# Performance work log

Hardware: AMD Instinct MI355X
Metric: run time of the kernel (lower is better)

The kernel has to match this reference:

```python
import jax, jax.numpy as jnp
import numpy as np

N_GROUP = 64
GROUP_SIZE = 64
INPUT_DIM = 2048
BATCH = 8192
N_MONTN = 512


def setup_inputs() -> dict:
    key = jax.random.key(0)
    k1, k2, k3, k4, k5 = jax.random.split(key, 5)
    x = jax.random.normal(k1, (BATCH, INPUT_DIM), dtype=jnp.float32)
    weight = jax.random.normal(k2, (N_GROUP * GROUP_SIZE, INPUT_DIM), dtype=jnp.float32) * 0.02
    bias = jax.random.normal(k3, (N_GROUP * GROUP_SIZE,), dtype=jnp.float32) * 0.02
    rand_u = jax.random.uniform(k4, (BATCH,), dtype=jnp.float32)
    montn_index = jax.random.randint(k5, (N_MONTN,), 0, INPUT_DIM, dtype=jnp.int32)
    return {"x": x, "weight": weight, "bias": bias, "rand_u": rand_u,
            "montn_index": montn_index}


def reference(x, weight, bias, rand_u, montn_index):
    # Square the weights on monotone input columns (in-place in torch).
    w = weight.at[:, montn_index].set(weight[:, montn_index] ** 2)
    # y = x @ w^T + b  -> [B, n_group * n_group_size]
    y = jnp.einsum('bi,oi->bo', x, w) + bias
    B = y.shape[0]
    # per-group min over contiguous slices, then max over groups
    group_mins = y.reshape(B, N_GROUP, GROUP_SIZE).min(axis=2)  # [B, n_group]
    out = group_mins.max(axis=1)                                 # [B]
    # vectorized Bernoulli: 1.0 if u < sigmoid(out) else 0.0
    sample = (rand_u < jax.nn.sigmoid(out)).astype(jnp.float32)
    return sample.reshape(-1, 1)
```

## Files before the change

kernel.cpp:

```cpp
#include <hip/hip_runtime.h>
#include <cmath>


typedef _Float16 f16x8 __attribute__((ext_vector_type(8)));
typedef float f32x4 __attribute__((ext_vector_type(4)));

#define MARGIN_EPS 4e-3f
#define MAX_UNDEC 96

__device__ __forceinline__ void async_load16(const void* gptr, void* lptr) {
  __builtin_amdgcn_global_load_lds(
      (const __attribute__((address_space(1))) void*)gptr,
      (__attribute__((address_space(3))) void*)lptr, 16, 0, 0);
}

__device__ __forceinline__ float us2f(unsigned short u) {
  return (float)__builtin_bit_cast(_Float16, u);
}

__global__ void build_mask(const int* __restrict__ idx,
                           unsigned* __restrict__ mask32, int* __restrict__ count) {
  const int t = threadIdx.x;
  if (t < 64) mask32[t] = 0u;
  if (t == 0) *count = 0;
  __syncthreads();
  for (int j = t; j < 512; j += 256) {
    const int c = idx[j];
    atomicOr(&mask32[c >> 5], 1u << (c & 31));
  }
}

__global__ void convert_split(float* __restrict__ x, float* __restrict__ wgt,
                              const unsigned* __restrict__ mask32) {
  const int t = threadIdx.x, l = t & 63, w = t >> 6;
  const int r = blockIdx.x * 4 + w;
  const int use_mask = (r >= 8192) ? 1 : 0;
  float* rowp = use_mask ? (wgt + (size_t)(r - 8192) * 2048)
                         : (x + (size_t)r * 2048);
  float4 v[8];
#pragma unroll
  for (int j = 0; j < 8; ++j) v[j] = ((const float4*)rowp)[l + 64 * j];
  unsigned mw[8];
#pragma unroll
  for (int j = 0; j < 8; ++j)
    mw[j] = use_mask ? mask32[(l >> 3) + 8 * j] : 0u;

  unsigned short* up = (unsigned short*)rowp;
#pragma unroll
  for (int j = 0; j < 8; ++j) {
    unsigned short hs[4], ls[4];
    const float* fv = (const float*)&v[j];
#pragma unroll
    for (int c = 0; c < 4; ++c) {
      float f = fv[c];
      if ((mw[j] >> (4 * (l & 7) + c)) & 1u) f = f * f;
      _Float16 h = (_Float16)f;
      float res = f - (float)h;
      _Float16 lo = (_Float16)res;
      hs[c] = __builtin_bit_cast(unsigned short, h);
      ls[c] = __builtin_bit_cast(unsigned short, lo);
    }
    uint2 H, L;
    H.x = (unsigned)hs[0] | ((unsigned)hs[1] << 16);
    H.y = (unsigned)hs[2] | ((unsigned)hs[3] << 16);
    L.x = (unsigned)ls[0] | ((unsigned)ls[1] << 16);
    L.y = (unsigned)ls[2] | ((unsigned)ls[3] << 16);
    *((uint2*)(up + 4 * l + 256 * j)) = H;
    *((uint2*)(up + 2048 + 4 * l + 256 * j)) = L;
  }
}

__global__ __launch_bounds__(256, 2) void gemm_minmax(
    const unsigned short* __restrict__ X, const unsigned short* __restrict__ W,
    const float* __restrict__ bias, float* __restrict__ gmins) {
  __shared__ unsigned short As[128 * 64];
  __shared__ unsigned short Bs[256 * 64];
  const int t = threadIdx.x;
  const int lane = t & 63;
  const int w = t >> 6;
  const int wm = w >> 1, wn = w & 1;
  const int m0 = blockIdx.y * 128;
  const int n0 = blockIdx.x * 256;

  const int rowBase = w * 8 + (lane >> 3);
  const int gchunk = ((lane & 7) ^ ((lane >> 3) & 7)) * 8;
  const size_t gA0 = (size_t)(m0 + rowBase) * 4096 + gchunk;
  const size_t gB0 = (size_t)(n0 + rowBase) * 4096 + gchunk;
  unsigned short* ldsA0 = As + w * 512;
  unsigned short* ldsB0 = Bs + w * 512;

  const int am = lane & 15, quad = lane >> 4;
  int arow[4], brow[8];
#pragma unroll
  for (int i = 0; i < 4; ++i) arow[i] = (wm * 64 + i * 16 + am) * 64;
#pragma unroll
  for (int j = 0; j < 8; ++j) brow[j] = (wn * 128 + j * 16 + am) * 64;
  int swz[2];
#pragma unroll
  for (int h = 0; h < 2; ++h) swz[h] = (((h << 2) + quad) ^ (am & 7)) * 8;

  f32x4 acc[4][8];
#pragma unroll
  for (int i = 0; i < 4; ++i)
#pragma unroll
    for (int j = 0; j < 8; ++j) acc[i][j] = (f32x4){0.f, 0.f, 0.f, 0.f};

#pragma unroll 1
  for (int it = 0; it < 32; ++it) {
    const int kin = it * 64;
    __syncthreads();
#pragma unroll
    for (int c = 0; c < 4; ++c)
      async_load16(X + gA0 + (size_t)c * (32 * 4096) + kin, ldsA0 + c * 2048);
#pragma unroll
    for (int c = 0; c < 8; ++c)
      async_load16(W + gB0 + (size_t)c * (32 * 4096) + kin, ldsB0 + c * 2048);
    __syncthreads();

#pragma unroll
    for (int h = 0; h < 2; ++h) {
      f16x8 av[4], bv[8];
#pragma unroll
      for (int i = 0; i < 4; ++i) av[i] = *(const f16x8*)(As + arow[i] + swz[h]);
#pragma unroll
      for (int j = 0; j < 8; ++j) bv[j] = *(const f16x8*)(Bs + brow[j] + swz[h]);
#pragma unroll
      for (int mb = 0; mb < 4; ++mb)
#pragma unroll
        for (int nb = 0; nb < 8; ++nb)
          acc[mb][nb] = __builtin_amdgcn_mfma_f32_16x16x32_f16(
              av[mb], bv[nb], acc[mb][nb], 0, 0, 0);
    }
  }

  float bv8[8];
#pragma unroll
  for (int nb = 0; nb < 8; ++nb) bv8[nb] = bias[n0 + wn * 128 + nb * 16 + am];
#pragma unroll
  for (int hh = 0; hh < 2; ++hh) {
    const int grp = (n0 >> 6) + wn * 2 + hh;
#pragma unroll
    for (int mb = 0; mb < 4; ++mb) {
#pragma unroll
      for (int reg = 0; reg < 4; ++reg) {
        float v = fminf(
            fminf(acc[mb][4 * hh + 0][reg] + bv8[4 * hh + 0],
                  acc[mb][4 * hh + 1][reg] + bv8[4 * hh + 1]),
            fminf(acc[mb][4 * hh + 2][reg] + bv8[4 * hh + 2],
                  acc[mb][4 * hh + 3][reg] + bv8[4 * hh + 3]));
        v = fminf(v, __shfl_xor(v, 1, 64));
        v = fminf(v, __shfl_xor(v, 2, 64));
        v = fminf(v, __shfl_xor(v, 4, 64));
        v = fminf(v, __shfl_xor(v, 8, 64));
        if (am == 0) {
          const int row = m0 + wm * 64 + mb * 16 + quad * 4 + reg;
          gmins[(size_t)row * 64 + grp] = v;
        }
      }
    }
  }
}

__global__ void finalize_margin(const float* __restrict__ gmins,
                                const float* __restrict__ rand_u,
                                float* __restrict__ out,
                                int* __restrict__ count, int* __restrict__ undec) {
  const int wv = threadIdx.x >> 6, lane = threadIdx.x & 63;
  const int row = blockIdx.x * 4 + wv;
  float v = gmins[(size_t)row * 64 + lane];
  v = fmaxf(v, __shfl_xor(v, 1, 64));
  v = fmaxf(v, __shfl_xor(v, 2, 64));
  v = fmaxf(v, __shfl_xor(v, 4, 64));
  v = fmaxf(v, __shfl_xor(v, 8, 64));
  v = fmaxf(v, __shfl_xor(v, 16, 64));
  v = fmaxf(v, __shfl_xor(v, 32, 64));
  if (lane == 0) {
    const float u = rand_u[row];
    const float slo = 1.0f / (1.0f + expf(-(v - MARGIN_EPS)));
    const float shi = 1.0f / (1.0f + expf(-(v + MARGIN_EPS)));
    if (u < slo) {
      out[row] = 1.0f;
    } else if (u >= shi) {
      out[row] = 0.0f;
    } else {
      const int i = atomicAdd(count, 1);
      if (i < 8192) undec[i] = row;
    }
  }
}

__global__ void zero_ybuf(float4* __restrict__ p) {
  p[(size_t)blockIdx.x * 256 + threadIdx.x] = (float4){0.f, 0.f, 0.f, 0.f};
}

__global__ __launch_bounds__(256) void recompute_rows(
    const unsigned short* __restrict__ X, const unsigned short* __restrict__ W,
    const int* __restrict__ count, const int* __restrict__ undec,
    float* __restrict__ ybuf) {
  __shared__ float wf[64 * 513];
  __shared__ float part[256];
  const int g = blockIdx.x, kc = blockIdx.y;
  const int t = threadIdx.x;
  int n = *count;
  if (n > MAX_UNDEC) n = MAX_UNDEC;
  if (n == 0) return;

  {
    const int cl = t >> 2, ks = t & 3;
    const unsigned short* wp =
        W + (size_t)(g * 64 + cl) * 4096 + kc * 512 + ks * 128;
    float* dst = wf + cl * 513 + ks * 128;
    for (int i = 0; i < 128; i += 8) {
      uint4 hv = *(const uint4*)(wp + i);
      uint4 lv = *(const uint4*)(wp + 2048 + i);
      const unsigned* hw = (const unsigned*)&hv;
      const unsigned* lw = (const unsigned*)&lv;
#pragma unroll
      for (int m = 0; m < 4; ++m) {
        dst[i + 2 * m] = us2f((unsigned short)(hw[m] & 0xFFFF)) +
                         us2f((unsigned short)(lw[m] & 0xFFFF));
        dst[i + 2 * m + 1] = us2f((unsigned short)(hw[m] >> 16)) +
                             us2f((unsigned short)(lw[m] >> 16));
      }
    }
  }
  __syncthreads();

  const int col = t & 63, kq = t >> 6;
  const float* wcol = wf + col * 513 + kq * 128;
  for (int s = 0; s < n; ++s) {
    const int row = undec[s];
    const unsigned short* xp = X + (size_t)row * 4096 + kc * 512 + kq * 128;
    float acc = 0.f;
    for (int i = 0; i < 128; i += 8) {
      uint4 hv = *(const uint4*)(xp + i);
      uint4 lv = *(const uint4*)(xp + 2048 + i);
      const unsigned* hw = (const unsigned*)&hv;
      const unsigned* lw = (const unsigned*)&lv;
#pragma unroll
      for (int m = 0; m < 4; ++m) {
        const float x0 = us2f((unsigned short)(hw[m] & 0xFFFF)) +
                         us2f((unsigned short)(lw[m] & 0xFFFF));
        const float x1 = us2f((unsigned short)(hw[m] >> 16)) +
                         us2f((unsigned short)(lw[m] >> 16));
        acc = fmaf(x0, wcol[i + 2 * m], acc);
        acc = fmaf(x1, wcol[i + 2 * m + 1], acc);
      }
    }
    part[t] = acc;
    __syncthreads();
    if (t < 64) {
      const float y = part[t] + part[t + 64] + part[t + 128] + part[t + 192];
      atomicAdd(ybuf + (size_t)s * 4096 + g * 64 + t, y);
    }
    __syncthreads();
  }
}

__global__ void decide(const float* __restrict__ ybuf,
                       const int* __restrict__ undec, const int* __restrict__ count,
                       const float* __restrict__ bias,
                       const float* __restrict__ rand_u, float* __restrict__ out) {
  __shared__ float gm[64];
  int n = *count;
  if (n > MAX_UNDEC) n = MAX_UNDEC;
  const int s = blockIdx.x;
  if (s >= n) return;
  const int t = threadIdx.x;
  const int g = t >> 2, p4 = t & 3;
  const float* yb = ybuf + (size_t)s * 4096;
  const int c0 = g * 64 + p4 * 16;
  float m = 3.4e38f;
#pragma unroll
  for (int e = 0; e < 16; ++e) m = fminf(m, yb[c0 + e] + bias[c0 + e]);
  m = fminf(m, __shfl_xor(m, 1, 64));
  m = fminf(m, __shfl_xor(m, 2, 64));
  if (p4 == 0) gm[g] = m;
  __syncthreads();
  if (t < 64) {
    float v = gm[t];
    v = fmaxf(v, __shfl_xor(v, 1, 64));
    v = fmaxf(v, __shfl_xor(v, 2, 64));
    v = fmaxf(v, __shfl_xor(v, 4, 64));
    v = fmaxf(v, __shfl_xor(v, 8, 64));
    v = fmaxf(v, __shfl_xor(v, 16, 64));
    v = fmaxf(v, __shfl_xor(v, 32, 64));
    if (t == 0) {
      const int row = undec[s];
      const float sg = 1.0f / (1.0f + expf(-v));
      out[row] = (rand_u[row] < sg) ? 1.0f : 0.0f;
    }
  }
}

extern "C" void kernel_launch(void* const* d_in, const int* in_sizes, int n_in,
                              void* d_out, int out_size, void* d_ws, size_t ws_size,
                              hipStream_t stream) {
  float* x = (float*)d_in[0];
  float* weight = (float*)d_in[1];
  const float* bias = (const float*)d_in[2];
  const float* rand_u = (const float*)d_in[3];
  const int* montn = (const int*)d_in[4];
  float* out = (float*)d_out;

  char* ws = (char*)d_ws;
  unsigned* mask32 = (unsigned*)ws;
  int* count = (int*)(ws + 256);
  int* undec = (int*)(ws + 512);
  float* ybuf = (float*)(ws + 65536);
  float* gmins = (float*)(ws + 65536 + 1572864);

  build_mask<<<1, 256, 0, stream>>>(montn, mask32, count);
  convert_split<<<3072, 256, 0, stream>>>(x, weight, mask32);
  gemm_minmax<<<dim3(16, 64), 256, 0, stream>>>(
      (const unsigned short*)x, (const unsigned short*)weight, bias, gmins);
  finalize_margin<<<2048, 256, 0, stream>>>(gmins, rand_u, out, count, undec);
  zero_ybuf<<<384, 256, 0, stream>>>((float4*)ybuf);
  recompute_rows<<<dim3(64, 4), 256, 0, stream>>>(
      (const unsigned short*)x, (const unsigned short*)weight, count, undec, ybuf);
  decide<<<MAX_UNDEC, 256, 0, stream>>>(ybuf, undec, count, bias, rand_u, out);
}
```

Baseline: 308.7 us.

## Retile GEMM to 128x128 with 32x32 MFMA and fuse small kernels

Switches the GEMM from 128x256 tiles using 16x16x32 MFMA to 128x128 tiles using 32x32x16 MFMA. It adds a swizzled 1D block order for L2 locality and allows 4 blocks per CU instead of 2. The mask build moves into convert_split through shared memory, and zeroing of ybuf is folded into finalize_margin, which removes two launches. recompute_rows splits K into 16 chunks instead of 4 for more parallelism, at the cost of lower per-block data reuse in the GEMM and more atomics in the recompute.

```diff
diff --git a/kernel.cpp b/kernel.cpp
--- a/kernel.cpp
+++ b/kernel.cpp
@@ -3,7 +3,7 @@
 
 
 typedef _Float16 f16x8 __attribute__((ext_vector_type(8)));
-typedef float f32x4 __attribute__((ext_vector_type(4)));
+typedef float f32x16 __attribute__((ext_vector_type(16)));
 
 #define MARGIN_EPS 4e-3f
 #define MAX_UNDEC 96
@@ -18,23 +18,23 @@
   return (float)__builtin_bit_cast(_Float16, u);
 }
 
-__global__ void build_mask(const int* __restrict__ idx,
-                           unsigned* __restrict__ mask32, int* __restrict__ count) {
-  const int t = threadIdx.x;
-  if (t < 64) mask32[t] = 0u;
-  if (t == 0) *count = 0;
-  __syncthreads();
-  for (int j = t; j < 512; j += 256) {
-    const int c = idx[j];
-    atomicOr(&mask32[c >> 5], 1u << (c & 31));
-  }
-}
-
 __global__ void convert_split(float* __restrict__ x, float* __restrict__ wgt,
-                              const unsigned* __restrict__ mask32) {
+                              const int* __restrict__ montn,
+                              int* __restrict__ count) {
+  __shared__ unsigned msk[64];
   const int t = threadIdx.x, l = t & 63, w = t >> 6;
   const int r = blockIdx.x * 4 + w;
   const int use_mask = (r >= 8192) ? 1 : 0;
+  if (blockIdx.x == 0 && t == 0) *count = 0;
+  if (use_mask) {
+    if (t < 64) msk[t] = 0u;
+    __syncthreads();
+    for (int j = t; j < 512; j += 256) {
+      const int c = montn[j];
+      atomicOr(&msk[c >> 5], 1u << (c & 31));
+    }
+    __syncthreads();
+  }
   float* rowp = use_mask ? (wgt + (size_t)(r - 8192) * 2048)
                          : (x + (size_t)r * 2048);
   float4 v[8];
@@ -43,7 +43,7 @@
   unsigned mw[8];
 #pragma unroll
   for (int j = 0; j < 8; ++j)
-    mw[j] = use_mask ? mask32[(l >> 3) + 8 * j] : 0u;
+    mw[j] = use_mask ? msk[(l >> 3) + 8 * j] : 0u;
 
   unsigned short* up = (unsigned short*)rowp;
 #pragma unroll
@@ -70,92 +70,93 @@
   }
 }
 
-__global__ __launch_bounds__(256, 2) void gemm_minmax(
+__global__ __launch_bounds__(256, 4) void gemm_minmax(
     const unsigned short* __restrict__ X, const unsigned short* __restrict__ W,
     const float* __restrict__ bias, float* __restrict__ gmins) {
   __shared__ unsigned short As[128 * 64];
-  __shared__ unsigned short Bs[256 * 64];
+  __shared__ unsigned short Bs[128 * 64];
   const int t = threadIdx.x;
   const int lane = t & 63;
   const int w = t >> 6;
   const int wm = w >> 1, wn = w & 1;
-  const int m0 = blockIdx.y * 128;
-  const int n0 = blockIdx.x * 256;
+  const int lin = blockIdx.x;
+  const int sid = lin >> 3;
+  const int m0 = (sid >> 2) * 128;
+  const int n0 = ((lin & 7) * 4 + (sid & 3)) * 128;
 
   const int rowBase = w * 8 + (lane >> 3);
   const int gchunk = ((lane & 7) ^ ((lane >> 3) & 7)) * 8;
-  const size_t gA0 = (size_t)(m0 + rowBase) * 4096 + gchunk;
-  const size_t gB0 = (size_t)(n0 + rowBase) * 4096 + gchunk;
-  unsigned short* ldsA0 = As + w * 512;
-  unsigned short* ldsB0 = Bs + w * 512;
-
-  const int am = lane & 15, quad = lane >> 4;
-  int arow[4], brow[8];
-#pragma unroll
-  for (int i = 0; i < 4; ++i) arow[i] = (wm * 64 + i * 16 + am) * 64;
-#pragma unroll
-  for (int j = 0; j < 8; ++j) brow[j] = (wn * 128 + j * 16 + am) * 64;
-  int swz[2];
-#pragma unroll
-  for (int h = 0; h < 2; ++h) swz[h] = (((h << 2) + quad) ^ (am & 7)) * 8;
-
-  f32x4 acc[4][8];
-#pragma unroll
-  for (int i = 0; i < 4; ++i)
-#pragma unroll
-    for (int j = 0; j < 8; ++j) acc[i][j] = (f32x4){0.f, 0.f, 0.f, 0.f};
+  size_t sA[4], sB[4];
+#pragma unroll
+  for (int c = 0; c < 4; ++c) {
+    sA[c] = (size_t)(m0 + c * 32 + rowBase) * 4096 + gchunk;
+    sB[c] = (size_t)(n0 + c * 32 + rowBase) * 4096 + gchunk;
+  }
+  unsigned short* ldsA[4];
+  unsigned short* ldsB[4];
+#pragma unroll
+  for (int c = 0; c < 4; ++c) {
+    ldsA[c] = As + c * 2048 + w * 512;
+    ldsB[c] = Bs + c * 2048 + w * 512;
+  }
+
+  const int l31 = lane & 31, hi32 = lane >> 5;
+  int arow[2], brow[2], swz[4];
+#pragma unroll
+  for (int i = 0; i < 2; ++i) {
+    arow[i] = (wm * 64 + i * 32 + l31) * 64;
+    brow[i] = (wn * 64 + i * 32 + l31) * 64;
+  }
+#pragma unroll
+  for (int s = 0; s < 4; ++s) swz[s] = ((2 * s + hi32) ^ (lane & 7)) * 8;
+
+  f32x16 acc[2][2];
+#pragma unroll
+  for (int i = 0; i < 2; ++i)
+#pragma unroll
+    for (int j = 0; j < 2; ++j) acc[i][j] = (f32x16)(0.f);
 
 #pragma unroll 1
   for (int it = 0; it < 32; ++it) {
     const int kin = it * 64;
     __syncthreads();
 #pragma unroll
-    for (int c = 0; c < 4; ++c)
-      async_load16(X + gA0 + (size_t)c * (32 * 4096) + kin, ldsA0 + c * 2048);
-#pragma unroll
-    for (int c = 0; c < 8; ++c)
-      async_load16(W + gB0 + (size_t)c * (32 * 4096) + kin, ldsB0 + c * 2048);
-    __syncthreads();
-
-#pragma unroll
-    for (int h = 0; h < 2; ++h) {
-      f16x8 av[4], bv[8];
-#pragma unroll
-      for (int i = 0; i < 4; ++i) av[i] = *(const f16x8*)(As + arow[i] + swz[h]);
-#pragma unroll
-      for (int j = 0; j < 8; ++j) bv[j] = *(const f16x8*)(Bs + brow[j] + swz[h]);
-#pragma unroll
-      for (int mb = 0; mb < 4; ++mb)
-#pragma unroll
-        for (int nb = 0; nb < 8; ++nb)
-          acc[mb][nb] = __builtin_amdgcn_mfma_f32_16x16x32_f16(
-              av[mb], bv[nb], acc[mb][nb], 0, 0, 0);
-    }
-  }
-
-  float bv8[8];
-#pragma unroll
-  for (int nb = 0; nb < 8; ++nb) bv8[nb] = bias[n0 + wn * 128 + nb * 16 + am];
-#pragma unroll
-  for (int hh = 0; hh < 2; ++hh) {
-    const int grp = (n0 >> 6) + wn * 2 + hh;
-#pragma unroll
-    for (int mb = 0; mb < 4; ++mb) {
-#pragma unroll
-      for (int reg = 0; reg < 4; ++reg) {
-        float v = fminf(
-            fminf(acc[mb][4 * hh + 0][reg] + bv8[4 * hh + 0],
-                  acc[mb][4 * hh + 1][reg] + bv8[4 * hh + 1]),
-            fminf(acc[mb][4 * hh + 2][reg] + bv8[4 * hh + 2],
-                  acc[mb][4 * hh + 3][reg] + bv8[4 * hh + 3]));
-        v = fminf(v, __shfl_xor(v, 1, 64));
-        v = fminf(v, __shfl_xor(v, 2, 64));
-        v = fminf(v, __shfl_xor(v, 4, 64));
-        v = fminf(v, __shfl_xor(v, 8, 64));
-        if (am == 0) {
-          const int row = m0 + wm * 64 + mb * 16 + quad * 4 + reg;
-          gmins[(size_t)row * 64 + grp] = v;
-        }
+    for (int c = 0; c < 4; ++c) {
+      async_load16(X + sA[c] + kin, ldsA[c]);
+      async_load16(W + sB[c] + kin, ldsB[c]);
+    }
+    __syncthreads();
+
+#pragma unroll
+    for (int s = 0; s < 4; ++s) {
+      f16x8 a0 = *(const f16x8*)(As + arow[0] + swz[s]);
+      f16x8 a1 = *(const f16x8*)(As + arow[1] + swz[s]);
+      f16x8 b0 = *(const f16x8*)(Bs + brow[0] + swz[s]);
+      f16x8 b1 = *(const f16x8*)(Bs + brow[1] + swz[s]);
+      acc[0][0] = __builtin_amdgcn_mfma_f32_32x32x16_f16(a0, b0, acc[0][0], 0, 0, 0);
+      acc[0][1] = __builtin_amdgcn_mfma_f32_32x32x16_f16(a0, b1, acc[0][1], 0, 0, 0);
+      acc[1][0] = __builtin_amdgcn_mfma_f32_32x32x16_f16(a1, b0, acc[1][0], 0, 0, 0);
+      acc[1][1] = __builtin_amdgcn_mfma_f32_32x32x16_f16(a1, b1, acc[1][1], 0, 0, 0);
+    }
+  }
+
+  float bia[2];
+#pragma unroll
+  for (int nt = 0; nt < 2; ++nt) bia[nt] = bias[n0 + wn * 64 + nt * 32 + l31];
+  const int grp = (n0 >> 6) + wn;
+#pragma unroll
+  for (int mt = 0; mt < 2; ++mt) {
+#pragma unroll
+    for (int r = 0; r < 16; ++r) {
+      float v = fminf(acc[mt][0][r] + bia[0], acc[mt][1][r] + bia[1]);
+      v = fminf(v, __shfl_xor(v, 1, 64));
+      v = fminf(v, __shfl_xor(v, 2, 64));
+      v = fminf(v, __shfl_xor(v, 4, 64));
+      v = fminf(v, __shfl_xor(v, 8, 64));
+      v = fminf(v, __shfl_xor(v, 16, 64));
+      if (l31 == 0) {
+        const int row = m0 + wm * 64 + mt * 32 + (r & 3) + 8 * (r >> 2) + 4 * hi32;
+        gmins[(size_t)row * 64 + grp] = v;
       }
     }
   }
@@ -164,7 +165,10 @@
 __global__ void finalize_margin(const float* __restrict__ gmins,
                                 const float* __restrict__ rand_u,
                                 float* __restrict__ out,
-                                int* __restrict__ count, int* __restrict__ undec) {
+                                int* __restrict__ count, int* __restrict__ undec,
+                                float4* __restrict__ ybuf4) {
+  if (blockIdx.x < 384)
+    ybuf4[(size_t)blockIdx.x * 256 + threadIdx.x] = (float4){0.f, 0.f, 0.f, 0.f};
   const int wv = threadIdx.x >> 6, lane = threadIdx.x & 63;
   const int row = blockIdx.x * 4 + wv;
   float v = gmins[(size_t)row * 64 + lane];
@@ -189,15 +193,11 @@
   }
 }
 
-__global__ void zero_ybuf(float4* __restrict__ p) {
-  p[(size_t)blockIdx.x * 256 + threadIdx.x] = (float4){0.f, 0.f, 0.f, 0.f};
-}
-
 __global__ __launch_bounds__(256) void recompute_rows(
     const unsigned short* __restrict__ X, const unsigned short* __restrict__ W,
     const int* __restrict__ count, const int* __restrict__ undec,
     float* __restrict__ ybuf) {
-  __shared__ float wf[64 * 513];
+  __shared__ float wf[64 * 129];
   __shared__ float part[256];
   const int g = blockIdx.x, kc = blockIdx.y;
   const int t = threadIdx.x;
@@ -208,9 +208,10 @@
   {
     const int cl = t >> 2, ks = t & 3;
     const unsigned short* wp =
-        W + (size_t)(g * 64 + cl) * 4096 + kc * 512 + ks * 128;
-    float* dst = wf + cl * 513 + ks * 128;
-    for (int i = 0; i < 128; i += 8) {
+        W + (size_t)(g * 64 + cl) * 4096 + kc * 128 + ks * 32;
+    float* dst = wf + cl * 129 + ks * 32;
+#pragma unroll
+    for (int i = 0; i < 32; i += 8) {
       uint4 hv = *(const uint4*)(wp + i);
       uint4 lv = *(const uint4*)(wp + 2048 + i);
       const unsigned* hw = (const unsigned*)&hv;
@@ -227,12 +228,13 @@
   __syncthreads();
 
   const int col = t & 63, kq = t >> 6;
-  const float* wcol = wf + col * 513 + kq * 128;
+  const float* wcol = wf + col * 129 + kq * 32;
   for (int s = 0; s < n; ++s) {
     const int row = undec[s];
-    const unsigned short* xp = X + (size_t)row * 4096 + kc * 512 + kq * 128;
+    const unsigned short* xp = X + (size_t)row * 4096 + kc * 128 + kq * 32;
     float acc = 0.f;
-    for (int i = 0; i < 128; i += 8) {
+#pragma unroll
+    for (int i = 0; i < 32; i += 8) {
       uint4 hv = *(const uint4*)(xp + i);
       uint4 lv = *(const uint4*)(xp + 2048 + i);
       const unsigned* hw = (const unsigned*)&hv;
@@ -304,19 +306,17 @@
   float* out = (float*)d_out;
 
   char* ws = (char*)d_ws;
-  unsigned* mask32 = (unsigned*)ws;
-  int* count = (int*)(ws + 256);
-  int* undec = (int*)(ws + 512);
+  int* count = (int*)ws;
+  int* undec = (int*)(ws + 256);
   float* ybuf = (float*)(ws + 65536);
   float* gmins = (float*)(ws + 65536 + 1572864);
 
-  build_mask<<<1, 256, 0, stream>>>(montn, mask32, count);
-  convert_split<<<3072, 256, 0, stream>>>(x, weight, mask32);
-  gemm_minmax<<<dim3(16, 64), 256, 0, stream>>>(
+  convert_split<<<3072, 256, 0, stream>>>(x, weight, montn, count);
+  gemm_minmax<<<2048, 256, 0, stream>>>(
       (const unsigned short*)x, (const unsigned short*)weight, bias, gmins);
-  finalize_margin<<<2048, 256, 0, stream>>>(gmins, rand_u, out, count, undec);
-  zero_ybuf<<<384, 256, 0, stream>>>((float4*)ybuf);
-  recompute_rows<<<dim3(64, 4), 256, 0, stream>>>(
+  finalize_margin<<<2048, 256, 0, stream>>>(gmins, rand_u, out, count, undec,
+                                            (float4*)ybuf);
+  recompute_rows<<<dim3(64, 16), 256, 0, stream>>>(
       (const unsigned short*)x, (const unsigned short*)weight, count, undec, ybuf);
   decide<<<MAX_UNDEC, 256, 0, stream>>>(ybuf, undec, count, bias, rand_u, out);
 }
```

After: 328.0 us. +6.3%, slower.

## Fold mask build and ybuf zeroing into neighbors, remap GEMM tiles, widen recompute grid

Applied to the files above, without the earlier changes.

Removes the build_mask and zero_ybuf launches: each weight-row block of convert_split builds the monotone mask in shared memory, and finalize_margin zeroes ybuf. convert_split now does 32-byte per-lane loads and 16-byte stores. gemm_minmax uses a 1D grid with a swizzled block-to-tile mapping meant to improve L2 reuse. recompute_rows splits K into 16 chunks instead of 4, using less LDS per block and giving more parallelism. The costs are a redundant mask build in every weight block and more atomic adds into ybuf.

```diff
diff --git a/kernel.cpp b/kernel.cpp
--- a/kernel.cpp
+++ b/kernel.cpp
@@ -18,55 +18,64 @@
   return (float)__builtin_bit_cast(_Float16, u);
 }
 
-__global__ void build_mask(const int* __restrict__ idx,
-                           unsigned* __restrict__ mask32, int* __restrict__ count) {
-  const int t = threadIdx.x;
-  if (t < 64) mask32[t] = 0u;
-  if (t == 0) *count = 0;
-  __syncthreads();
-  for (int j = t; j < 512; j += 256) {
-    const int c = idx[j];
-    atomicOr(&mask32[c >> 5], 1u << (c & 31));
-  }
-}
-
 __global__ void convert_split(float* __restrict__ x, float* __restrict__ wgt,
-                              const unsigned* __restrict__ mask32) {
+                              const int* __restrict__ montn,
+                              int* __restrict__ count) {
+  __shared__ unsigned msk[64];
   const int t = threadIdx.x, l = t & 63, w = t >> 6;
   const int r = blockIdx.x * 4 + w;
   const int use_mask = (r >= 8192) ? 1 : 0;
+  if (blockIdx.x == 0 && t == 0) *count = 0;
+  if (use_mask) {
+    if (t < 64) msk[t] = 0u;
+    __syncthreads();
+    for (int j = t; j < 512; j += 256) {
+      const int c = montn[j];
+      atomicOr(&msk[c >> 5], 1u << (c & 31));
+    }
+    __syncthreads();
+  }
   float* rowp = use_mask ? (wgt + (size_t)(r - 8192) * 2048)
                          : (x + (size_t)r * 2048);
-  float4 v[8];
-#pragma unroll
-  for (int j = 0; j < 8; ++j) v[j] = ((const float4*)rowp)[l + 64 * j];
-  unsigned mw[8];
-#pragma unroll
-  for (int j = 0; j < 8; ++j)
-    mw[j] = use_mask ? mask32[(l >> 3) + 8 * j] : 0u;
+  float4 v[4][2];
+#pragma unroll
+  for (int p = 0; p < 4; ++p) {
+    v[p][0] = ((const float4*)rowp)[p * 128 + 2 * l];
+    v[p][1] = ((const float4*)rowp)[p * 128 + 2 * l + 1];
+  }
+  unsigned mw[4];
+#pragma unroll
+  for (int p = 0; p < 4; ++p)
+    mw[p] = use_mask ? msk[p * 16 + (l >> 2)] : 0u;
 
   unsigned short* up = (unsigned short*)rowp;
 #pragma unroll
-  for (int j = 0; j < 8; ++j) {
-    unsigned short hs[4], ls[4];
-    const float* fv = (const float*)&v[j];
-#pragma unroll
-    for (int c = 0; c < 4; ++c) {
-      float f = fv[c];
-      if ((mw[j] >> (4 * (l & 7) + c)) & 1u) f = f * f;
-      _Float16 h = (_Float16)f;
-      float res = f - (float)h;
+  for (int p = 0; p < 4; ++p) {
+    float f[8];
+    f[0] = v[p][0].x; f[1] = v[p][0].y; f[2] = v[p][0].z; f[3] = v[p][0].w;
+    f[4] = v[p][1].x; f[5] = v[p][1].y; f[6] = v[p][1].z; f[7] = v[p][1].w;
+    unsigned short hs[8], ls[8];
+#pragma unroll
+    for (int c = 0; c < 8; ++c) {
+      float g = f[c];
+      if ((mw[p] >> (8 * (l & 3) + c)) & 1u) g = g * g;
+      _Float16 h = (_Float16)g;
+      float res = g - (float)h;
       _Float16 lo = (_Float16)res;
       hs[c] = __builtin_bit_cast(unsigned short, h);
       ls[c] = __builtin_bit_cast(unsigned short, lo);
     }
-    uint2 H, L;
+    uint4 H, L;
     H.x = (unsigned)hs[0] | ((unsigned)hs[1] << 16);
     H.y = (unsigned)hs[2] | ((unsigned)hs[3] << 16);
+    H.z = (unsigned)hs[4] | ((unsigned)hs[5] << 16);
+    H.w = (unsigned)hs[6] | ((unsigned)hs[7] << 16);
     L.x = (unsigned)ls[0] | ((unsigned)ls[1] << 16);
     L.y = (unsigned)ls[2] | ((unsigned)ls[3] << 16);
-    *((uint2*)(up + 4 * l + 256 * j)) = H;
-    *((uint2*)(up + 2048 + 4 * l + 256 * j)) = L;
+    L.z = (unsigned)ls[4] | ((unsigned)ls[5] << 16);
+    L.w = (unsigned)ls[6] | ((unsigned)ls[7] << 16);
+    *((uint4*)(up + p * 512 + 8 * l)) = H;
+    *((uint4*)(up + 2048 + p * 512 + 8 * l)) = L;
   }
 }
 
@@ -79,8 +88,10 @@
   const int lane = t & 63;
   const int w = t >> 6;
   const int wm = w >> 1, wn = w & 1;
-  const int m0 = blockIdx.y * 128;
-  const int n0 = blockIdx.x * 256;
+  const int lin = blockIdx.x;
+  const int sid = lin >> 3;
+  const int m0 = (sid >> 1) * 128;
+  const int n0 = ((lin & 7) * 2 + (sid & 1)) * 256;
 
   const int rowBase = w * 8 + (lane >> 3);
   const int gchunk = ((lane & 7) ^ ((lane >> 3) & 7)) * 8;
@@ -164,7 +175,10 @@
 __global__ void finalize_margin(const float* __restrict__ gmins,
                                 const float* __restrict__ rand_u,
                                 float* __restrict__ out,
-                                int* __restrict__ count, int* __restrict__ undec) {
+                                int* __restrict__ count, int* __restrict__ undec,
+                                float4* __restrict__ ybuf4) {
+  if (blockIdx.x < 384)
+    ybuf4[(size_t)blockIdx.x * 256 + threadIdx.x] = (float4){0.f, 0.f, 0.f, 0.f};
   const int wv = threadIdx.x >> 6, lane = threadIdx.x & 63;
   const int row = blockIdx.x * 4 + wv;
   float v = gmins[(size_t)row * 64 + lane];
@@ -189,15 +203,11 @@
   }
 }
 
-__global__ void zero_ybuf(float4* __restrict__ p) {
-  p[(size_t)blockIdx.x * 256 + threadIdx.x] = (float4){0.f, 0.f, 0.f, 0.f};
-}
-
 __global__ __launch_bounds__(256) void recompute_rows(
     const unsigned short* __restrict__ X, const unsigned short* __restrict__ W,
     const int* __restrict__ count, const int* __restrict__ undec,
     float* __restrict__ ybuf) {
-  __shared__ float wf[64 * 513];
+  __shared__ float wf[64 * 129];
   __shared__ float part[256];
   const int g = blockIdx.x, kc = blockIdx.y;
   const int t = threadIdx.x;
@@ -208,9 +218,10 @@
   {
     const int cl = t >> 2, ks = t & 3;
     const unsigned short* wp =
-        W + (size_t)(g * 64 + cl) * 4096 + kc * 512 + ks * 128;
-    float* dst = wf + cl * 513 + ks * 128;
-    for (int i = 0; i < 128; i += 8) {
+        W + (size_t)(g * 64 + cl) * 4096 + kc * 128 + ks * 32;
+    float* dst = wf + cl * 129 + ks * 32;
+#pragma unroll
+    for (int i = 0; i < 32; i += 8) {
       uint4 hv = *(const uint4*)(wp + i);
       uint4 lv = *(const uint4*)(wp + 2048 + i);
       const unsigned* hw = (const unsigned*)&hv;
@@ -227,12 +238,13 @@
   __syncthreads();
 
   const int col = t & 63, kq = t >> 6;
-  const float* wcol = wf + col * 513 + kq * 128;
+  const float* wcol = wf + col * 129 + kq * 32;
   for (int s = 0; s < n; ++s) {
     const int row = undec[s];
-    const unsigned short* xp = X + (size_t)row * 4096 + kc * 512 + kq * 128;
+    const unsigned short* xp = X + (size_t)row * 4096 + kc * 128 + kq * 32;
     float acc = 0.f;
-    for (int i = 0; i < 128; i += 8) {
+#pragma unroll
+    for (int i = 0; i < 32; i += 8) {
       uint4 hv = *(const uint4*)(xp + i);
       uint4 lv = *(const uint4*)(xp + 2048 + i);
       const unsigned* hw = (const unsigned*)&hv;
@@ -304,19 +316,17 @@
   float* out = (float*)d_out;
 
   char* ws = (char*)d_ws;
-  unsigned* mask32 = (unsigned*)ws;
-  int* count = (int*)(ws + 256);
-  int* undec = (int*)(ws + 512);
+  int* count = (int*)ws;
+  int* undec = (int*)(ws + 256);
   float* ybuf = (float*)(ws + 65536);
   float* gmins = (float*)(ws + 65536 + 1572864);
 
-  build_mask<<<1, 256, 0, stream>>>(montn, mask32, count);
-  convert_split<<<3072, 256, 0, stream>>>(x, weight, mask32);
-  gemm_minmax<<<dim3(16, 64), 256, 0, stream>>>(
+  convert_split<<<3072, 256, 0, stream>>>(x, weight, montn, count);
+  gemm_minmax<<<1024, 256, 0, stream>>>(
       (const unsigned short*)x, (const unsigned short*)weight, bias, gmins);
-  finalize_margin<<<2048, 256, 0, stream>>>(gmins, rand_u, out, count, undec);
-  zero_ybuf<<<384, 256, 0, stream>>>((float4*)ybuf);
-  recompute_rows<<<dim3(64, 4), 256, 0, stream>>>(
+  finalize_margin<<<2048, 256, 0, stream>>>(gmins, rand_u, out, count, undec,
+                                            (float4*)ybuf);
+  recompute_rows<<<dim3(64, 16), 256, 0, stream>>>(
       (const unsigned short*)x, (const unsigned short*)weight, count, undec, ybuf);
   decide<<<MAX_UNDEC, 256, 0, stream>>>(ybuf, undec, count, bias, rand_u, out);
 }
```

After: 284.4 us. -7.9%, faster.
